# Kernel tuning notes

Measured on AMD Instinct MI355X. Metric: run time of the kernel, lower is better.

The kernel has to match this reference:

```python
import jax, jax.numpy as jnp
import numpy as np

B, S, H = 64, 512, 768
N_SPANS, MAX_SPAN, CW = 4, 8, 3
NH = 8
HD = H // NH
W = MAX_SPAN + 1 + 2 * CW  # max context window length (15)
H2 = H // 2
N_ATE, N_SENT = 2, 2


def _ln(x, g, b, eps=1e-5):
    m = x.mean(-1, keepdims=True)
    v = ((x - m) ** 2).mean(-1, keepdims=True)
    return (x - m) / jnp.sqrt(v + eps) * g + b


def _classifier(x, w1, b1, g, bb, w2, b2):
    # Dropout -> Linear -> GELU -> LayerNorm -> Linear (eval mode: dropout = id)
    h = jax.nn.gelu(x @ w1.T + b1, approximate=False)
    h = _ln(h, g, bb)
    return h @ w2.T + b2


def setup_inputs() -> dict:
    key = jax.random.key(0)
    ks = jax.random.split(key, 16)
    p = lambda k, shape: (0.02 * jax.random.normal(k, shape)).astype(jnp.float32)
    seq_out = jax.random.normal(ks[0], (B, S, H), dtype=jnp.float32)
    starts = jax.random.randint(ks[1], (B, N_SPANS), 1, S - MAX_SPAN - 1)
    lens = jax.random.randint(ks[2], (B, N_SPANS), 1, MAX_SPAN + 1)
    ends = starts + lens  # exclusive end, span length in [1, MAX_SPAN]
    return dict(
        seq_out=seq_out,
        span_starts=starts.astype(jnp.int32),
        span_ends=ends.astype(jnp.int32),
        ate_g=jnp.ones((H,), jnp.float32), ate_b=jnp.zeros((H,), jnp.float32),
        apc_g=jnp.ones((H,), jnp.float32), apc_b=jnp.zeros((H,), jnp.float32),
        w_in=p(ks[3], (3 * H, H)), b_in=jnp.zeros((3 * H,), jnp.float32),
        w_out=p(ks[4], (H, H)), b_out=jnp.zeros((H,), jnp.float32),
        fus_w=p(ks[5], (H, 2 * H)), fus_b=jnp.zeros((H,), jnp.float32),
        asp_w1=p(ks[6], (H2, H)), asp_b1=jnp.zeros((H2,), jnp.float32),
        asp_lng=jnp.ones((H2,), jnp.float32), asp_lnb=jnp.zeros((H2,), jnp.float32),
        asp_w2=p(ks[7], (N_ATE, H2)), asp_b2=jnp.zeros((N_ATE,), jnp.float32),
        sen_w1=p(ks[8], (H2, H)), sen_b1=jnp.zeros((H2,), jnp.float32),
        sen_lng=jnp.ones((H2,), jnp.float32), sen_lnb=jnp.zeros((H2,), jnp.float32),
        sen_w2=p(ks[9], (N_SENT, H2)), sen_b2=jnp.zeros((N_SENT,), jnp.float32),
    )


def _fwd(seq_out, ate_g, ate_b, apc_g, apc_b, w_in, b_in, w_out, b_out,
         fus_w, fus_b, asp_w1, asp_b1, asp_lng, asp_lnb, asp_w2, asp_b2,
         sen_w1, sen_b1, sen_lng, sen_lnb, sen_w2, sen_b2,
         span_starts, span_ends):
    dt = seq_out.dtype
    # clamping semantics as in the torch loop
    s = jnp.clip(span_starts, 0, S - 1)
    e = jnp.maximum(s, jnp.minimum(span_ends, S - 1))
    left = jnp.maximum(0, s - CW)
    right = jnp.minimum(S, e + 1 + CW)

    # ATE head over all tokens
    ate_logits = _classifier(_ln(seq_out, ate_g, ate_b),
                             asp_w1, asp_b1, asp_lng, asp_lnb, asp_w2, asp_b2)

    gather = jax.vmap(lambda so, idx: so[idx])  # ([S,H],[N,W]) -> [N,W,H]

    # aspect mean over tokens [s, e)
    aidx = s[..., None] + jnp.arange(MAX_SPAN)          # [B,N,MS]
    va = (aidx < e[..., None]).astype(dt)
    asp_tok = gather(seq_out, jnp.clip(aidx, 0, S - 1)) # [B,N,MS,H]
    cnt = va.sum(-1, keepdims=True)                     # [B,N,1]
    asp_mean = (asp_tok * va[..., None]).sum(-2) / jnp.maximum(cnt, 1.0)
    asp_mean = jnp.where(cnt > 0, asp_mean, seq_out[:, None, 0, :])

    # context window [left, right): tiny self-attention, then mean
    cidx = left[..., None] + jnp.arange(W)              # [B,N,W]
    vc = (cidx < right[..., None]).astype(dt)
    ctx = gather(seq_out, jnp.clip(cidx, 0, S - 1))     # [B,N,W,H]
    qkv = ctx @ w_in.T + b_in
    q, k, v = jnp.split(qkv, 3, axis=-1)
    q = q.reshape(B, N_SPANS, W, NH, HD) * (HD ** -0.5)
    k = k.reshape(B, N_SPANS, W, NH, HD)
    v = v.reshape(B, N_SPANS, W, NH, HD)
    scores = jnp.einsum('bnqhd,bnkhd->bnhqk', q, k)
    neg = jnp.asarray(jnp.finfo(dt).min, dt)
    scores = jnp.where(vc[:, :, None, None, :] > 0, scores, neg)
    attn = jax.nn.softmax(scores, axis=-1)
    out = jnp.einsum('bnhqk,bnkhd->bnqhd', attn, v).reshape(B, N_SPANS, W, H)
    out = out @ w_out.T + b_out
    ccnt = vc.sum(-1, keepdims=True)
    ctx_mean = (out * vc[..., None]).sum(-2) / jnp.maximum(ccnt, 1.0)

    combined = jnp.concatenate([asp_mean, ctx_mean], axis=-1)  # [B,N,2H]
    fused = jax.nn.gelu(combined @ fus_w.T + fus_b, approximate=False)
    apc_feat = fused.mean(axis=1)                              # [B,H]
    apc_logits = _classifier(_ln(apc_feat, apc_g, apc_b),
                             sen_w1, sen_b1, sen_lng, sen_lnb, sen_w2, sen_b2)
    return ate_logits, apc_logits


def reference(seq_out, span_starts, span_ends, ate_g, ate_b, apc_g, apc_b,
              w_in, b_in, w_out, b_out, fus_w, fus_b,
              asp_w1, asp_b1, asp_lng, asp_lnb, asp_w2, asp_b2,
              sen_w1, sen_b1, sen_lng, sen_lnb, sen_w2, sen_b2):
    return _fwd(seq_out, ate_g, ate_b, apc_g, apc_b, w_in, b_in, w_out, b_out,
                fus_w, fus_b, asp_w1, asp_b1, asp_lng, asp_lnb, asp_w2, asp_b2,
                sen_w1, sen_b1, sen_lng, sen_lnb, sen_w2, sen_b2,
                span_starts, span_ends)
```

## Files before the change

### kernel.cpp

```cpp
#include <hip/hip_runtime.h>
#include <math.h>

#define DEVI __device__ __forceinline__

using bf16x8 = __attribute__((ext_vector_type(8))) short;
using f32x4  = __attribute__((ext_vector_type(4))) float;

DEVI float b2f(unsigned short u) {
  union { unsigned int u; float f; } x; x.u = ((unsigned int)u) << 16; return x.f;
}
DEVI unsigned short f2b(float f) {
  union { float f; unsigned int u; } x; x.f = f;
  unsigned int r = (x.u + 0x7fffu + ((x.u >> 16) & 1u)) >> 16;
  return (unsigned short)r;
}
DEVI float gelu_f(float x) { return 0.5f * x * (1.0f + erff(x * 0.70710678118654752440f)); }

DEVI void wredxor2(float& a, float& b) {
  #pragma unroll
  for (int off = 32; off; off >>= 1) {
    a += __shfl_xor(a, off);
    b += __shfl_xor(b, off);
  }
}

template<int NW>
DEVI void breduce2(float& a, float& b) {
  __shared__ float buf[2 * NW];
  int lane = threadIdx.x & 63;
  int w = threadIdx.x >> 6;
  #pragma unroll
  for (int off = 32; off > 0; off >>= 1) {
    a += __shfl_down(a, off);
    b += __shfl_down(b, off);
  }
  if (lane == 0) { buf[w] = a; buf[NW + w] = b; }
  __syncthreads();
  float ra = 0.f, rb = 0.f;
  #pragma unroll
  for (int i = 0; i < NW; ++i) { ra += buf[i]; rb += buf[NW + i]; }
  a = ra; b = rb;
  __syncthreads();
}

DEVI void span_params(const int* st, const int* en, int span,
                      int& s, int& e, int& left, int& right) {
  int s0 = st[span], e0 = en[span];
  s = min(max(s0, 0), 511);
  e = max(s, min(e0, 511));
  left = max(0, s - 3);
  right = min(512, e + 4);
}

DEVI int xcd_logical(int bid, int n) {
  int q = n >> 3, r = n & 7;
  int xcd = bid & 7, idx = bid >> 3;
  return (xcd < r ? xcd * (q + 1) : r * (q + 1) + (xcd - r) * q) + idx;
}

__global__ __launch_bounds__(256) void prep_kernel(
    const float* __restrict__ w1, const float* __restrict__ w_in,
    const float* __restrict__ w_out, const float* __restrict__ fus_w,
    const float* __restrict__ sen_w1,
    unsigned short* __restrict__ d0, unsigned short* __restrict__ d1,
    unsigned short* __restrict__ d2, unsigned short* __restrict__ d3,
    unsigned short* __restrict__ d4,
    const float* __restrict__ seq, const float* __restrict__ ate_g,
    const float* __restrict__ ate_b, unsigned short* __restrict__ sbf,
    float2* __restrict__ stats, float2* __restrict__ c12,
    const int* __restrict__ st, const int* __restrict__ en,
    int* __restrict__ tokmap) {
  const int bid = blockIdx.x, tid = threadIdx.x;
  if (bid < 4032) {
    int i = bid * 256 + tid;
    if (i < 73728) {
      float4 v = reinterpret_cast<const float4*>(w1)[i];
      int k0 = (i * 4) % 768;
      float4 gv = *reinterpret_cast<const float4*>(ate_g + k0);
      ushort4 o;
      o.x = f2b(v.x * gv.x); o.y = f2b(v.y * gv.y);
      o.z = f2b(v.z * gv.z); o.w = f2b(v.w * gv.w);
      reinterpret_cast<ushort4*>(d0)[i] = o;
      return;
    }
    const float* s; unsigned short* d; int j;
    if (i < 516096)      { s = w_in;   d = d1; j = i - 73728; }
    else if (i < 663552) { s = w_out;  d = d2; j = i - 516096; }
    else if (i < 958464) { s = fus_w;  d = d3; j = i - 663552; }
    else                 { s = sen_w1; d = d4; j = i - 958464; }
    float4 v = reinterpret_cast<const float4*>(s)[j];
    ushort4 o;
    o.x = f2b(v.x); o.y = f2b(v.y); o.z = f2b(v.z); o.w = f2b(v.w);
    reinterpret_cast<ushort4*>(d)[j] = o;
  } else if (bid < 12224) {
    const int row = (bid - 4032) * 4 + (tid >> 6);
    const int lane = tid & 63;
    const float4* xr = reinterpret_cast<const float4*>(seq + (size_t)row * 768);
    float4 v[3];
    #pragma unroll
    for (int j = 0; j < 3; ++j) v[j] = xr[j * 64 + lane];
    float s = 0.f, q = 0.f;
    #pragma unroll
    for (int j = 0; j < 3; ++j) {
      s += v[j].x + v[j].y + v[j].z + v[j].w;
      q += v[j].x * v[j].x + v[j].y * v[j].y + v[j].z * v[j].z + v[j].w * v[j].w;
    }
    wredxor2(s, q);
    float mean = s * (1.0f / 768.0f);
    float rstd = rsqrtf(q * (1.0f / 768.0f) - mean * mean + 1e-5f);
    ushort4* orow = reinterpret_cast<ushort4*>(sbf + (size_t)row * 768);
    #pragma unroll
    for (int j = 0; j < 3; ++j) {
      ushort4 o;
      o.x = f2b(v[j].x); o.y = f2b(v[j].y); o.z = f2b(v[j].z); o.w = f2b(v[j].w);
      orow[j * 64 + lane] = o;
    }
    if (lane == 0) stats[row] = make_float2(rstd, rstd * mean);
  } else if (bid < 12320) {
    const int lane = tid & 63;
    const int j = (bid - 12224) * 4 + (tid >> 6);
    const float4* wr = reinterpret_cast<const float4*>(w1 + (size_t)j * 768);
    const float4* gp = reinterpret_cast<const float4*>(ate_g);
    const float4* bp = reinterpret_cast<const float4*>(ate_b);
    float a = 0.f, bsum = 0.f;
    #pragma unroll
    for (int i = 0; i < 3; ++i) {
      float4 wv = wr[i * 64 + lane];
      float4 gv = gp[i * 64 + lane];
      float4 bv = bp[i * 64 + lane];
      a    += gv.x * wv.x + gv.y * wv.y + gv.z * wv.z + gv.w * wv.w;
      bsum += bv.x * wv.x + bv.y * wv.y + bv.z * wv.z + bv.w * wv.w;
    }
    wredxor2(a, bsum);
    if (lane == 0) c12[j] = make_float2(a, bsum);
  } else {
    for (int i = tid; i < 3840; i += 256) {
      int span = i / 15, w = i % 15;
      int s, e, left, right;
      span_params(st, en, span, s, e, left, right);
      int b = span >> 2;
      tokmap[i] = b * 512 + min(left + w, 511);
    }
  }
}

template<int BM, int BN, int WM, int WN>
DEVI void gemm_core(const unsigned short* __restrict__ A,
                    const unsigned short* __restrict__ W,
                    int K, int bm, int bn,
                    unsigned short* As, unsigned short* Bs,
                    f32x4 (&acc)[WM / 16][WN / 16],
                    const int* __restrict__ rowmap = nullptr) {
  constexpr int CA = BM / 8;
  constexpr int CB = BN / 8;
  constexpr int NWC = BN / WN;
  constexpr int WAVES = (BM / WM) * NWC;
  constexpr int CPA = CA / WAVES;
  constexpr int CPB = CB / WAVES;
  constexpr int FM = WM / 16, FN = WN / 16;
  const int tid = threadIdx.x;
  const int lane = tid & 63;
  const int wv = tid >> 6;
  const int wr = wv / NWC, wc = wv % NWC;
  const int l16 = lane & 15, lhi = lane >> 4;
  const int srow = lane >> 3;
  const int scol = 8 * ((lane & 7) ^ srow);

  size_t aoff[CPA], boff[CPB];
  #pragma unroll
  for (int c = 0; c < CPA; ++c) {
    int ar = bm + (wv + c * WAVES) * 8 + srow;
    aoff[c] = (rowmap ? (size_t)rowmap[ar] : (size_t)ar) * K + scol;
  }
  #pragma unroll
  for (int c = 0; c < CPB; ++c)
    boff[c] = (size_t)(bn + (wv + c * WAVES) * 8 + srow) * K + scol;

  const int nt = K / 64;
  for (int t = 0; t < nt; ++t) {
    const int k0 = t * 64;
    #pragma unroll
    for (int c = 0; c < CPA; ++c)
      __builtin_amdgcn_global_load_lds(
          (const __attribute__((address_space(1))) void*)&A[aoff[c] + k0],
          (__attribute__((address_space(3))) void*)&As[(wv + c * WAVES) * 512], 16, 0, 0);
    #pragma unroll
    for (int c = 0; c < CPB; ++c)
      __builtin_amdgcn_global_load_lds(
          (const __attribute__((address_space(1))) void*)&W[boff[c] + k0],
          (__attribute__((address_space(3))) void*)&Bs[(wv + c * WAVES) * 512], 16, 0, 0);
    __syncthreads();
    #pragma unroll
    for (int kk = 0; kk < 2; ++kk) {
      bf16x8 af[FM], bfr[FN];
      #pragma unroll
      for (int fm = 0; fm < FM; ++fm) {
        int r = wr * WM + fm * 16 + l16;
        af[fm] = *reinterpret_cast<const bf16x8*>(&As[r * 64 + ((kk * 32 + lhi * 8) ^ ((r & 7) * 8))]);
      }
      #pragma unroll
      for (int fn = 0; fn < FN; ++fn) {
        int r = wc * WN + fn * 16 + l16;
        bfr[fn] = *reinterpret_cast<const bf16x8*>(&Bs[r * 64 + ((kk * 32 + lhi * 8) ^ ((r & 7) * 8))]);
      }
      #pragma unroll
      for (int fm = 0; fm < FM; ++fm)
        #pragma unroll
        for (int fn = 0; fn < FN; ++fn)
          acc[fm][fn] = __builtin_amdgcn_mfma_f32_16x16x32_bf16(af[fm], bfr[fn], acc[fm][fn], 0, 0, 0);
    }
    __syncthreads();
  }
}

template<int BM, int BN, int WM, int WN>
DEVI void gemm_store(const float* __restrict__ bias, unsigned short* __restrict__ C,
                     int NSTRIDE, bool act, int bm, int bn, f32x4 (&acc)[WM / 16][WN / 16]) {
  constexpr int NWC = BN / WN;
  constexpr int FM = WM / 16, FN = WN / 16;
  const int lane = threadIdx.x & 63;
  const int wv = threadIdx.x >> 6;
  const int wr = wv / NWC, wc = wv % NWC;
  const int l16 = lane & 15, lhi = lane >> 4;
  #pragma unroll
  for (int fm = 0; fm < FM; ++fm) {
    #pragma unroll
    for (int fn = 0; fn < FN; ++fn) {
      int col = bn + wc * WN + fn * 16 + l16;
      float bv = bias[col];
      #pragma unroll
      for (int i = 0; i < 4; ++i) {
        int row = bm + wr * WM + fm * 16 + lhi * 4 + i;
        float v = acc[fm][fn][i] + bv;
        if (act) v = gelu_f(v);
        C[(size_t)row * NSTRIDE + col] = f2b(v);
      }
    }
  }
}

template<int BM, int BN, int WM, int WN, int ACT>
__global__ __launch_bounds__(256) void gemm_swz64(
    const unsigned short* __restrict__ A, const unsigned short* __restrict__ W,
    const float* __restrict__ bias, unsigned short* __restrict__ C,
    int M, int NSTRIDE, int K, int nbN) {
  __shared__ __align__(16) unsigned short As[BM * 64];
  __shared__ __align__(16) unsigned short Bs[BN * 64];
  int l = xcd_logical(blockIdx.x, gridDim.x);
  int mb = l / nbN, nb = l % nbN;
  f32x4 acc[WM / 16][WN / 16] = {};
  gemm_core<BM, BN, WM, WN>(A, W, K, mb * BM, nb * BN, As, Bs, acc);
  gemm_store<BM, BN, WM, WN>(bias, C, NSTRIDE, ACT != 0, mb * BM, nb * BN, acc);
}

__global__ __launch_bounds__(512) void dual_gemm_kernel(
    const unsigned short* __restrict__ sbf, const unsigned short* __restrict__ w1b,
    const float* __restrict__ b1, const float2* __restrict__ c12,
    const float2* __restrict__ stats, const float* __restrict__ lng,
    const float* __restrict__ w2, float4* __restrict__ hpart,
    const unsigned short* __restrict__ winb, const float* __restrict__ b_in,
    unsigned short* __restrict__ qkv, const int* __restrict__ tokmap) {
  __shared__ __align__(16) unsigned short lds[384 * 64];
  if (blockIdx.x < 384) {
    int l = xcd_logical(blockIdx.x, 384);
    int mb = l / 3, nb = l % 3;
    const int bm = mb * 256, bn = nb * 128;
    f32x4 acc[4][4] = {};
    gemm_core<256, 128, 64, 64>(sbf, w1b, 768, bm, bn, lds, lds + 256 * 64, acc);
    const int lane = threadIdx.x & 63;
    const int wv = threadIdx.x >> 6;
    const int wr = wv >> 1, wc = wv & 1;
    const int l16 = lane & 15, lhi = lane >> 4;
    float b1v[4], gw2a[4], gw2b[4], c1v[4], c2v[4];
    #pragma unroll
    for (int fn = 0; fn < 4; ++fn) {
      int col = bn + wc * 64 + fn * 16 + l16;
      b1v[fn] = b1[col];
      float2 cc = c12[col];
      c1v[fn] = cc.x; c2v[fn] = cc.y;
      float gg = lng[col];
      gw2a[fn] = gg * w2[col];
      gw2b[fn] = gg * w2[384 + col];
    }
    #pragma unroll
    for (int fm = 0; fm < 4; ++fm) {
      #pragma unroll
      for (int i = 0; i < 4; ++i) {
        int row = bm + wr * 64 + fm * 16 + lhi * 4 + i;
        float2 sr = stats[row];
        float s1 = 0.f, s2 = 0.f, q0 = 0.f, q1 = 0.f;
        #pragma unroll
        for (int fn = 0; fn < 4; ++fn) {
          float h = gelu_f(sr.x * acc[fm][fn][i] - sr.y * c1v[fn] + c2v[fn] + b1v[fn]);
          s1 += h; s2 += h * h;
          q0 += h * gw2a[fn]; q1 += h * gw2b[fn];
        }
        #pragma unroll
        for (int off = 1; off < 16; off <<= 1) {
          s1 += __shfl_xor(s1, off); s2 += __shfl_xor(s2, off);
          q0 += __shfl_xor(q0, off); q1 += __shfl_xor(q1, off);
        }
        if (l16 == 0) hpart[(size_t)row * 6 + nb * 2 + wc] = make_float4(s1, s2, q0, q1);
      }
    }
  } else {
    int bid = blockIdx.x - 384;
    int l = xcd_logical(bid, 270);
    int mb = l / 9, nb = l % 9;
    f32x4 acc[4][4] = {};
    gemm_core<128, 256, 64, 64>(sbf, winb, 768, mb * 128, nb * 256,
                                lds, lds + 128 * 64, acc, tokmap);
    gemm_store<128, 256, 64, 64>(b_in, qkv, 2304, false, mb * 128, nb * 256, acc);
  }
}

__global__ __launch_bounds__(256) void finattn_kernel(
    const float4* __restrict__ hpart, const float* __restrict__ lng,
    const float* __restrict__ lnb, const float* __restrict__ w2,
    const float* __restrict__ b2, float* __restrict__ out,
    const unsigned short* __restrict__ qkv, const int* __restrict__ st,
    const int* __restrict__ en, unsigned short* __restrict__ cavg,
    const unsigned short* __restrict__ sbf, unsigned short* __restrict__ comb) {
  const int tid = threadIdx.x;
  if (blockIdx.x >= 2176) {
    const int span = blockIdx.x - 2176;
    int s, e, left, right;
    span_params(st, en, span, s, e, left, right);
    int b = span >> 2;
    int e2 = min(e, s + 8);
    int cnt = e2 - s;
    float inva = (cnt > 0) ? 1.0f / (float)cnt : 0.f;
    for (int c = tid; c < 768; c += 256) {
      float sa = 0.f;
      for (int t = s; t < e2; ++t) sa += b2f(sbf[((size_t)b * 512 + t) * 768 + c]);
      float asp = (cnt > 0) ? sa * inva : b2f(sbf[((size_t)b * 512) * 768 + c]);
      comb[(size_t)span * 1536 + c] = f2b(asp);
    }
    return;
  }
  if (blockIdx.x >= 2048) {
    __shared__ float cbuf[16];
    float c1a = 0.f, c1b = 0.f, c2a = 0.f, c2b = 0.f;
    for (int c = tid; c < 384; c += 256) {
      float gg = lng[c], bbv = lnb[c], wa = w2[c], wb = w2[384 + c];
      c1a += gg * wa; c1b += gg * wb;
      c2a += bbv * wa; c2b += bbv * wb;
    }
    wredxor2(c1a, c1b);
    wredxor2(c2a, c2b);
    if ((tid & 63) == 0) {
      int w = tid >> 6;
      cbuf[w * 4] = c1a; cbuf[w * 4 + 1] = c1b;
      cbuf[w * 4 + 2] = c2a; cbuf[w * 4 + 3] = c2b;
    }
    __syncthreads();
    c1a = cbuf[0] + cbuf[4] + cbuf[8] + cbuf[12];
    c1b = cbuf[1] + cbuf[5] + cbuf[9] + cbuf[13];
    c2a = cbuf[2] + cbuf[6] + cbuf[10] + cbuf[14];
    c2b = cbuf[3] + cbuf[7] + cbuf[11] + cbuf[15];
    const int row = (blockIdx.x - 2048) * 256 + tid;
    float S1 = 0.f, S2 = 0.f, D0 = 0.f, D1 = 0.f;
    #pragma unroll
    for (int p = 0; p < 6; ++p) {
      float4 v = hpart[(size_t)row * 6 + p];
      S1 += v.x; S2 += v.y; D0 += v.z; D1 += v.w;
    }
    float mu = S1 * (1.f / 384.f);
    float rstd = rsqrtf(S2 * (1.f / 384.f) - mu * mu + 1e-5f);
    out[(size_t)row * 2]     = rstd * (D0 - mu * c1a) + c2a + b2[0];
    out[(size_t)row * 2 + 1] = rstd * (D1 - mu * c1b) + c2b + b2[1];
    return;
  }
  __shared__ float qs[15][96], ks[15][96], vs[15][96];
  __shared__ float sc[15][16];
  __shared__ float wsum[15];
  const int span = blockIdx.x >> 3, hh = blockIdx.x & 7;
  int s, e, left, right;
  span_params(st, en, span, s, e, left, right);
  const int nv = right - left;
  const int r0 = span * 15;
  const float scale = 0.10206207261596576f;
  if (tid < 180) {
    int w = tid / 12, dp = tid % 12, d = dp * 8;
    const unsigned short* rowp = qkv + (size_t)(r0 + w) * 2304 + hh * 96 + d;
    bf16x8 qv = *reinterpret_cast<const bf16x8*>(rowp);
    bf16x8 kv = *reinterpret_cast<const bf16x8*>(rowp + 768);
    bf16x8 vv = *reinterpret_cast<const bf16x8*>(rowp + 1536);
    #pragma unroll
    for (int j = 0; j < 8; ++j) {
      qs[w][d + j] = b2f((unsigned short)qv[j]) * scale;
      ks[w][d + j] = b2f((unsigned short)kv[j]);
      vs[w][d + j] = b2f((unsigned short)vv[j]);
    }
  }
  __syncthreads();
  if (tid < 225) {
    int i = tid / 15, j = tid % 15;
    float a = 0.f;
    #pragma unroll
    for (int d = 0; d < 96; ++d) a += qs[i][d] * ks[j][d];
    sc[i][j] = (j < nv) ? a : -3.402823466e38f;
  }
  __syncthreads();
  if (tid < 15) {
    int i = tid;
    float m = -3.402823466e38f;
    #pragma unroll
    for (int j = 0; j < 15; ++j) m = fmaxf(m, sc[i][j]);
    float ex[15];
    float ssum = 0.f;
    #pragma unroll
    for (int j = 0; j < 15; ++j) { ex[j] = expf(sc[i][j] - m); ssum += ex[j]; }
    float inv = 1.0f / ssum;
    #pragma unroll
    for (int j = 0; j < 15; ++j) sc[i][j] = ex[j] * inv;
  }
  __syncthreads();
  if (tid < 15) {
    int j = tid;
    float a = 0.f;
    for (int i = 0; i < nv; ++i) a += sc[i][j];
    wsum[j] = a;
  }
  __syncthreads();
  if (tid < 96) {
    int d = tid;
    float r = 0.f;
    #pragma unroll
    for (int j = 0; j < 15; ++j) r += wsum[j] * vs[j][d];
    cavg[(size_t)span * 768 + hh * 96 + d] = f2b(r / (float)nv);
  }
}

__global__ __launch_bounds__(256) void apc_all_kernel(
    const unsigned short* __restrict__ fused, const float* __restrict__ g,
    const float* __restrict__ bb, const unsigned short* __restrict__ senb,
    const float* __restrict__ b1, const float* __restrict__ lng,
    const float* __restrict__ lnb, const float* __restrict__ w2,
    const float* __restrict__ b2, float* __restrict__ out) {
  const int b = blockIdx.x, tid = threadIdx.x;
  __shared__ float xs[768];
  __shared__ float hs[384];
  float v[3];
  #pragma unroll
  for (int j = 0; j < 3; ++j) {
    int c = tid + j * 256;
    float a = 0.f;
    #pragma unroll
    for (int n = 0; n < 4; ++n) a += b2f(fused[((size_t)(b * 4 + n)) * 768 + c]);
    v[j] = 0.25f * a;
  }
  float s = v[0] + v[1] + v[2];
  float q = v[0] * v[0] + v[1] * v[1] + v[2] * v[2];
  breduce2<4>(s, q);
  float mean = s * (1.f / 768.f);
  float rstd = rsqrtf(q * (1.f / 768.f) - mean * mean + 1e-5f);
  #pragma unroll
  for (int j = 0; j < 3; ++j) {
    int c = tid + j * 256;
    xs[c] = (v[j] - mean) * rstd * g[c] + bb[c];
  }
  __syncthreads();
  for (int j = tid; j < 384; j += 256) {
    const bf16x8* wrp = reinterpret_cast<const bf16x8*>(senb + (size_t)j * 768);
    float dot = 0.f;
    #pragma unroll 4
    for (int k8 = 0; k8 < 96; ++k8) {
      bf16x8 wv = wrp[k8];
      #pragma unroll
      for (int u = 0; u < 8; ++u) dot += xs[k8 * 8 + u] * b2f((unsigned short)wv[u]);
    }
    hs[j] = gelu_f(dot + b1[j]);
  }
  __syncthreads();
  s = 0.f; q = 0.f;
  for (int j = tid; j < 384; j += 256) { float h = hs[j]; s += h; q += h * h; }
  breduce2<4>(s, q);
  mean = s * (1.f / 384.f);
  rstd = rsqrtf(q * (1.f / 384.f) - mean * mean + 1e-5f);
  float p0 = 0.f, p1 = 0.f;
  for (int j = tid; j < 384; j += 256) {
    float hl = (hs[j] - mean) * rstd * lng[j] + lnb[j];
    p0 += hl * w2[j];
    p1 += hl * w2[384 + j];
  }
  breduce2<4>(p0, p1);
  if (tid == 0) {
    out[b * 2]     = p0 + b2[0];
    out[b * 2 + 1] = p1 + b2[1];
  }
}

extern "C" void kernel_launch(void* const* d_in, const int* in_sizes, int n_in,
                              void* d_out, int out_size, void* d_ws, size_t ws_size,
                              hipStream_t stream) {
  const float* seq    = (const float*)d_in[0];
  const int*   st     = (const int*)d_in[1];
  const int*   en     = (const int*)d_in[2];
  const float* ate_g  = (const float*)d_in[3];
  const float* ate_b  = (const float*)d_in[4];
  const float* apc_g  = (const float*)d_in[5];
  const float* apc_b  = (const float*)d_in[6];
  const float* w_in   = (const float*)d_in[7];
  const float* b_in   = (const float*)d_in[8];
  const float* w_out  = (const float*)d_in[9];
  const float* b_out  = (const float*)d_in[10];
  const float* fus_w  = (const float*)d_in[11];
  const float* fus_b  = (const float*)d_in[12];
  const float* asp_w1 = (const float*)d_in[13];
  const float* asp_b1 = (const float*)d_in[14];
  const float* asp_lng= (const float*)d_in[15];
  const float* asp_lnb= (const float*)d_in[16];
  const float* asp_w2 = (const float*)d_in[17];
  const float* asp_b2 = (const float*)d_in[18];
  const float* sen_w1 = (const float*)d_in[19];
  const float* sen_b1 = (const float*)d_in[20];
  const float* sen_lng= (const float*)d_in[21];
  const float* sen_lnb= (const float*)d_in[22];
  const float* sen_w2 = (const float*)d_in[23];
  const float* sen_b2 = (const float*)d_in[24];
  float* out = (float*)d_out;

  char* wsb = (char*)d_ws;
  unsigned short* sbf   = (unsigned short*)(wsb + 0);
  float2*        stats  = (float2*)(wsb + 50331648);
  float2*        c12    = (float2*)(wsb + 50593792);
  int*           tokmap = (int*)(wsb + 50596864);
  unsigned short* qkvb  = (unsigned short*)(wsb + 50612224);
  unsigned short* cavg  = (unsigned short*)(wsb + 68306944);
  unsigned short* comb  = (unsigned short*)(wsb + 68700160);
  unsigned short* fusO  = (unsigned short*)(wsb + 69486592);
  float4*        hpart  = (float4*)(wsb + 69879808);
  const size_t off_w = 73025536;
  unsigned short* w1b   = (unsigned short*)(wsb + off_w);
  unsigned short* winb  = (unsigned short*)(wsb + off_w + 589824);
  unsigned short* woutb = (unsigned short*)(wsb + off_w + 4128768);
  unsigned short* fusb  = (unsigned short*)(wsb + off_w + 5308416);
  unsigned short* senb  = (unsigned short*)(wsb + off_w + 7667712);

  prep_kernel<<<12321, 256, 0, stream>>>(asp_w1, w_in, w_out, fus_w, sen_w1,
                                         w1b, winb, woutb, fusb, senb,
                                         seq, ate_g, ate_b, sbf, stats, c12,
                                         st, en, tokmap);
  dual_gemm_kernel<<<654, 512, 0, stream>>>(sbf, w1b, asp_b1, c12, stats,
                                            asp_lng, asp_w2, hpart,
                                            winb, b_in, qkvb, tokmap);
  finattn_kernel<<<2432, 256, 0, stream>>>(hpart, asp_lng, asp_lnb, asp_w2, asp_b2, out,
                                           qkvb, st, en, cavg, sbf, comb);
  gemm_swz64<64, 128, 32, 64, 0><<<24, 256, 0, stream>>>(
      cavg, woutb, b_out, comb + 768, 256, 1536, 768, 6);
  gemm_swz64<64, 64, 32, 32, 1><<<48, 256, 0, stream>>>(
      comb, fusb, fus_b, fusO, 256, 768, 1536, 12);
  apc_all_kernel<<<64, 256, 0, stream>>>(fusO, apc_g, apc_b, senb, sen_b1,
                                         sen_lng, sen_lnb, sen_w2, sen_b2, out + 65536);
}
```

Baseline: 161.7 us.

## Fold out-projection weight into fusion weight to drop a GEMM launch

Precomputes a combined weight (fus_w right half times w_out) and a merged bias, so the context-mean path writes attention averages directly into the combined buffer and the separate out-projection GEMM kernel is removed. The weight product is computed as extra blocks inside the dual GEMM kernel, with a transposed w_out prepared in the prep kernel. This saves one kernel launch and a small GEMM on activations but adds a 768x768x768 weight GEMM and a transpose each call, plus extra bf16 rounding of the folded weight.

```diff
diff --git a/kernel.cpp b/kernel.cpp
--- a/kernel.cpp
+++ b/kernel.cpp
@@ -61,17 +61,19 @@
 __global__ __launch_bounds__(256) void prep_kernel(
     const float* __restrict__ w1, const float* __restrict__ w_in,
     const float* __restrict__ w_out, const float* __restrict__ fus_w,
-    const float* __restrict__ sen_w1,
-    unsigned short* __restrict__ d0, unsigned short* __restrict__ d1,
-    unsigned short* __restrict__ d2, unsigned short* __restrict__ d3,
-    unsigned short* __restrict__ d4,
+    const float* __restrict__ sen_w1, const float* __restrict__ fus_b,
+    const float* __restrict__ b_out,
+    unsigned short* __restrict__ w1b, unsigned short* __restrict__ winb,
+    unsigned short* __restrict__ Wbig, unsigned short* __restrict__ fusbR,
+    unsigned short* __restrict__ senb, unsigned short* __restrict__ w_outT,
+    float* __restrict__ bias2,
     const float* __restrict__ seq, const float* __restrict__ ate_g,
     const float* __restrict__ ate_b, unsigned short* __restrict__ sbf,
     float2* __restrict__ stats, float2* __restrict__ c12,
     const int* __restrict__ st, const int* __restrict__ en,
     int* __restrict__ tokmap) {
   const int bid = blockIdx.x, tid = threadIdx.x;
-  if (bid < 4032) {
+  if (bid < 3456) {
     int i = bid * 256 + tid;
     if (i < 73728) {
       float4 v = reinterpret_cast<const float4*>(w1)[i];
@@ -80,20 +82,36 @@
       ushort4 o;
       o.x = f2b(v.x * gv.x); o.y = f2b(v.y * gv.y);
       o.z = f2b(v.z * gv.z); o.w = f2b(v.w * gv.w);
-      reinterpret_cast<ushort4*>(d0)[i] = o;
+      reinterpret_cast<ushort4*>(w1b)[i] = o;
       return;
     }
-    const float* s; unsigned short* d; int j;
-    if (i < 516096)      { s = w_in;   d = d1; j = i - 73728; }
-    else if (i < 663552) { s = w_out;  d = d2; j = i - 516096; }
-    else if (i < 958464) { s = fus_w;  d = d3; j = i - 663552; }
-    else                 { s = sen_w1; d = d4; j = i - 958464; }
-    float4 v = reinterpret_cast<const float4*>(s)[j];
+    if (i < 516096) {
+      int j = i - 73728;
+      float4 v = reinterpret_cast<const float4*>(w_in)[j];
+      ushort4 o;
+      o.x = f2b(v.x); o.y = f2b(v.y); o.z = f2b(v.z); o.w = f2b(v.w);
+      reinterpret_cast<ushort4*>(winb)[j] = o;
+      return;
+    }
+    if (i < 811008) {
+      int j = i - 516096;
+      float4 v = reinterpret_cast<const float4*>(fus_w)[j];
+      ushort4 o;
+      o.x = f2b(v.x); o.y = f2b(v.y); o.z = f2b(v.z); o.w = f2b(v.w);
+      int row = j / 384, col4 = j % 384;
+      if (col4 < 192)
+        reinterpret_cast<ushort4*>(Wbig)[row * 384 + col4] = o;
+      else
+        reinterpret_cast<ushort4*>(fusbR)[row * 192 + (col4 - 192)] = o;
+      return;
+    }
+    int j = i - 811008;
+    float4 v = reinterpret_cast<const float4*>(sen_w1)[j];
     ushort4 o;
     o.x = f2b(v.x); o.y = f2b(v.y); o.z = f2b(v.z); o.w = f2b(v.w);
-    reinterpret_cast<ushort4*>(d)[j] = o;
-  } else if (bid < 12224) {
-    const int row = (bid - 4032) * 4 + (tid >> 6);
+    reinterpret_cast<ushort4*>(senb)[j] = o;
+  } else if (bid < 11648) {
+    const int row = (bid - 3456) * 4 + (tid >> 6);
     const int lane = tid & 63;
     const float4* xr = reinterpret_cast<const float4*>(seq + (size_t)row * 768);
     float4 v[3];
@@ -116,9 +134,9 @@
       orow[j * 64 + lane] = o;
     }
     if (lane == 0) stats[row] = make_float2(rstd, rstd * mean);
-  } else if (bid < 12320) {
+  } else if (bid < 11744) {
     const int lane = tid & 63;
-    const int j = (bid - 12224) * 4 + (tid >> 6);
+    const int j = (bid - 11648) * 4 + (tid >> 6);
     const float4* wr = reinterpret_cast<const float4*>(w1 + (size_t)j * 768);
     const float4* gp = reinterpret_cast<const float4*>(ate_g);
     const float4* bp = reinterpret_cast<const float4*>(ate_b);
@@ -133,6 +151,33 @@
     }
     wredxor2(a, bsum);
     if (lane == 0) c12[j] = make_float2(a, bsum);
+  } else if (bid < 11936) {
+    const int lane = tid & 63;
+    const int o = (bid - 11744) * 4 + (tid >> 6);
+    const float4* wr = reinterpret_cast<const float4*>(fus_w + (size_t)o * 1536 + 768);
+    const float4* bp = reinterpret_cast<const float4*>(b_out);
+    float a = 0.f, dummy = 0.f;
+    #pragma unroll
+    for (int i = 0; i < 3; ++i) {
+      float4 wv = wr[i * 64 + lane];
+      float4 bv = bp[i * 64 + lane];
+      a += wv.x * bv.x + wv.y * bv.y + wv.z * bv.z + wv.w * bv.w;
+    }
+    wredxor2(a, dummy);
+    if (lane == 0) bias2[o] = fus_b[o] + a;
+  } else if (bid < 11960) {
+    __shared__ unsigned short ldsT[32 * 770];
+    const int c0 = (bid - 11936) * 32;
+    for (int it = 0; it < 96; ++it) {
+      int j = it * 8 + (tid >> 5);
+      int c = tid & 31;
+      ldsT[c * 770 + j] = f2b(w_out[(size_t)j * 768 + c0 + c]);
+    }
+    __syncthreads();
+    for (int c = 0; c < 32; ++c) {
+      for (int u = tid; u < 768; u += 256)
+        w_outT[(size_t)(c0 + c) * 768 + u] = ldsT[c * 770 + u];
+    }
   } else {
     for (int i = tid; i < 3840; i += 256) {
       int span = i / 15, w = i % 15;
@@ -227,7 +272,7 @@
     #pragma unroll
     for (int fn = 0; fn < FN; ++fn) {
       int col = bn + wc * WN + fn * 16 + l16;
-      float bv = bias[col];
+      float bv = bias ? bias[col] : 0.f;
       #pragma unroll
       for (int i = 0; i < 4; ++i) {
         int row = bm + wr * WM + fm * 16 + lhi * 4 + i;
@@ -259,7 +304,9 @@
     const float2* __restrict__ stats, const float* __restrict__ lng,
     const float* __restrict__ w2, float4* __restrict__ hpart,
     const unsigned short* __restrict__ winb, const float* __restrict__ b_in,
-    unsigned short* __restrict__ qkv, const int* __restrict__ tokmap) {
+    unsigned short* __restrict__ qkv, const int* __restrict__ tokmap,
+    const unsigned short* __restrict__ fusbR, const unsigned short* __restrict__ w_outT,
+    unsigned short* __restrict__ Wbig) {
   __shared__ __align__(16) unsigned short lds[384 * 64];
   if (blockIdx.x < 384) {
     int l = xcd_logical(blockIdx.x, 384);
@@ -303,7 +350,7 @@
         if (l16 == 0) hpart[(size_t)row * 6 + nb * 2 + wc] = make_float4(s1, s2, q0, q1);
       }
     }
-  } else {
+  } else if (blockIdx.x < 654) {
     int bid = blockIdx.x - 384;
     int l = xcd_logical(bid, 270);
     int mb = l / 9, nb = l % 9;
@@ -311,6 +358,14 @@
     gemm_core<128, 256, 64, 64>(sbf, winb, 768, mb * 128, nb * 256,
                                 lds, lds + 128 * 64, acc, tokmap);
     gemm_store<128, 256, 64, 64>(b_in, qkv, 2304, false, mb * 128, nb * 256, acc);
+  } else {
+    if (threadIdx.x >= 256) return;
+    int l = blockIdx.x - 654;
+    int mb = l / 6, nb = l % 6;
+    f32x4 acc[4][4] = {};
+    gemm_core<128, 128, 64, 64>(fusbR, w_outT, 768, mb * 128, nb * 128,
+                                lds, lds + 128 * 64, acc);
+    gemm_store<128, 128, 64, 64>(nullptr, Wbig + 768, 1536, false, mb * 128, nb * 128, acc);
   }
 }
 
@@ -319,8 +374,8 @@
     const float* __restrict__ lnb, const float* __restrict__ w2,
     const float* __restrict__ b2, float* __restrict__ out,
     const unsigned short* __restrict__ qkv, const int* __restrict__ st,
-    const int* __restrict__ en, unsigned short* __restrict__ cavg,
-    const unsigned short* __restrict__ sbf, unsigned short* __restrict__ comb) {
+    const int* __restrict__ en, const unsigned short* __restrict__ sbf,
+    unsigned short* __restrict__ comb) {
   const int tid = threadIdx.x;
   if (blockIdx.x >= 2176) {
     const int span = blockIdx.x - 2176;
@@ -428,7 +483,7 @@
     float r = 0.f;
     #pragma unroll
     for (int j = 0; j < 15; ++j) r += wsum[j] * vs[j][d];
-    cavg[(size_t)span * 768 + hh * 96 + d] = f2b(r / (float)nv);
+    comb[(size_t)span * 1536 + 768 + hh * 96 + d] = f2b(r / (float)nv);
   }
 }
 
@@ -527,30 +582,31 @@
   float2*        c12    = (float2*)(wsb + 50593792);
   int*           tokmap = (int*)(wsb + 50596864);
   unsigned short* qkvb  = (unsigned short*)(wsb + 50612224);
-  unsigned short* cavg  = (unsigned short*)(wsb + 68306944);
-  unsigned short* comb  = (unsigned short*)(wsb + 68700160);
-  unsigned short* fusO  = (unsigned short*)(wsb + 69486592);
-  float4*        hpart  = (float4*)(wsb + 69879808);
-  const size_t off_w = 73025536;
+  unsigned short* comb  = (unsigned short*)(wsb + 68306944);
+  unsigned short* fusO  = (unsigned short*)(wsb + 69093376);
+  float4*        hpart  = (float4*)(wsb + 69486592);
+  const size_t off_w = 72632320;
   unsigned short* w1b   = (unsigned short*)(wsb + off_w);
   unsigned short* winb  = (unsigned short*)(wsb + off_w + 589824);
-  unsigned short* woutb = (unsigned short*)(wsb + off_w + 4128768);
-  unsigned short* fusb  = (unsigned short*)(wsb + off_w + 5308416);
-  unsigned short* senb  = (unsigned short*)(wsb + off_w + 7667712);
-
-  prep_kernel<<<12321, 256, 0, stream>>>(asp_w1, w_in, w_out, fus_w, sen_w1,
-                                         w1b, winb, woutb, fusb, senb,
+  unsigned short* w_outT= (unsigned short*)(wsb + off_w + 4128768);
+  unsigned short* Wbig  = (unsigned short*)(wsb + off_w + 5308416);
+  unsigned short* fusbR = (unsigned short*)(wsb + off_w + 7667712);
+  unsigned short* senb  = (unsigned short*)(wsb + off_w + 8847360);
+  float*         bias2  = (float*)(wsb + off_w + 9437184);
+
+  prep_kernel<<<11961, 256, 0, stream>>>(asp_w1, w_in, w_out, fus_w, sen_w1,
+                                         fus_b, b_out,
+                                         w1b, winb, Wbig, fusbR, senb, w_outT, bias2,
                                          seq, ate_g, ate_b, sbf, stats, c12,
                                          st, en, tokmap);
-  dual_gemm_kernel<<<654, 512, 0, stream>>>(sbf, w1b, asp_b1, c12, stats,
+  dual_gemm_kernel<<<690, 512, 0, stream>>>(sbf, w1b, asp_b1, c12, stats,
                                             asp_lng, asp_w2, hpart,
-                                            winb, b_in, qkvb, tokmap);
+                                            winb, b_in, qkvb, tokmap,
+                                            fusbR, w_outT, Wbig);
   finattn_kernel<<<2432, 256, 0, stream>>>(hpart, asp_lng, asp_lnb, asp_w2, asp_b2, out,
-                                           qkvb, st, en, cavg, sbf, comb);
-  gemm_swz64<64, 128, 32, 64, 0><<<24, 256, 0, stream>>>(
-      cavg, woutb, b_out, comb + 768, 256, 1536, 768, 6);
+                                           qkvb, st, en, sbf, comb);
   gemm_swz64<64, 64, 32, 32, 1><<<48, 256, 0, stream>>>(
-      comb, fusb, fus_b, fusO, 256, 768, 1536, 12);
+      comb, Wbig, bias2, fusO, 256, 768, 1536, 12);
   apc_all_kernel<<<64, 256, 0, stream>>>(fusO, apc_g, apc_b, senb, sen_b1,
                                          sen_lng, sen_lnb, sen_w2, sen_b2, out + 65536);
 }
```

Result: no change. 159.2 us (-1.5%).
